# Performance work log

Measured on AMD Instinct MI355X. Metric: run time of the kernel, lower is better.

Reference implementation:

```python
import jax, jax.numpy as jnp
import numpy as np

N = 100000
D = 64
H = 4 * D  # 256
E = 1000000


def setup_inputs() -> dict:
    key = jax.random.key(0)
    ks = jax.random.split(key, 9)
    return {
        "loc_feat": jax.random.normal(ks[0], (N, D), dtype=jnp.float32),
        "geo_src": jax.random.randint(ks[1], (E,), 0, N),
        "geo_dst": jax.random.randint(ks[2], (E,), 0, N),
        "trans_src": jax.random.randint(ks[3], (E,), 0, N),
        "trans_dst": jax.random.randint(ks[4], (E,), 0, N),
        "trans_w": jax.random.uniform(ks[5], (E,), dtype=jnp.float32),
        "W1": jax.random.normal(ks[6], (D, H), dtype=jnp.float32) * (1.0 / np.sqrt(D)),
        "b1": jax.random.normal(ks[7], (H,), dtype=jnp.float32) * 0.01,
        "W2": jax.random.normal(ks[8], (H, 1), dtype=jnp.float32) * (1.0 / np.sqrt(H)),
    }


def reference(loc_feat, geo_src, geo_dst, trans_src, trans_dst, trans_w, W1, b1, W2):
    n = loc_feat.shape[0]
    # etype 'geo': copy_u + mean  -> segment mean of src features at dst
    geo_sum = jax.ops.segment_sum(loc_feat[geo_src], geo_dst, num_segments=n)
    cnt = jax.ops.segment_sum(jnp.ones(geo_src.shape[0], loc_feat.dtype), geo_dst, num_segments=n)
    geo = jnp.where(cnt[:, None] > 0, geo_sum / jnp.maximum(cnt, 1.0)[:, None], 0.0)
    # etype 'trans': u_mul_e + sum -> weighted segment sum
    trans = jax.ops.segment_sum(loc_feat[trans_src] * trans_w[:, None], trans_dst, num_segments=n)
    # semantic attention fuse over the two relation views
    z = jnp.stack([geo, trans], axis=1)          # [N, 2, D]
    h = jnp.tanh(jnp.einsum('nkd,dh->nkh', z, W1) + b1)  # [N, 2, H]
    w = jnp.einsum('nkh,ho->nko', h, W2).mean(0)  # [2, 1] (mean over nodes)
    beta = jax.nn.softmax(w, axis=0)              # [2, 1]
    return (beta[None, :, :] * z).sum(1)          # [N, D]
```

## Files before the change

### kernel.cpp

```cpp
#include <hip/hip_runtime.h>
#include <hip/hip_bf16.h>

#define N_NODES 100000
#define DIM 64
#define HID 256
#define E_EDGES 1000000
#define TWO_N (2 * N_NODES)
#define MLP_ROWBLOCKS (TWO_N / 64)

#define TILE 240
#define NBINS 417
#define CAP 3072
#define EPB 4096
#define GEO_BLOCKS 245

typedef short short8 __attribute__((ext_vector_type(8)));
typedef float f32x4 __attribute__((ext_vector_type(4)));
typedef unsigned short us4 __attribute__((ext_vector_type(4)));

__device__ __forceinline__ float tanh_fast(float x) {
    x = fminf(fmaxf(x, -15.0f), 15.0f);
    float e = __expf(2.0f * x);
    return (e - 1.0f) / (e + 1.0f);
}

__device__ __forceinline__ unsigned short f2bf(float x) {
    unsigned u = __float_as_uint(x);
    u = u + 0x7FFFu + ((u >> 16) & 1u);
    return (unsigned short)(u >> 16);
}

__global__ void pack_feat_kernel(const float* __restrict__ feat,
                                 unsigned short* __restrict__ fb) {
    int i = blockIdx.x * 256 + threadIdx.x;
    float4 v = ((const float4*)feat)[i];
    us4 o;
    o[0] = f2bf(v.x); o[1] = f2bf(v.y); o[2] = f2bf(v.z); o[3] = f2bf(v.w);
    ((us4*)fb)[i] = o;
}

__global__ void bin_fill_kernel(const int* __restrict__ gs, const int* __restrict__ gd,
                                const int* __restrict__ ts, const int* __restrict__ td,
                                const float* __restrict__ tw,
                                int* __restrict__ gcount,
                                int* __restrict__ gbin, int2* __restrict__ tbin) {
    __shared__ int hist[NBINS];
    __shared__ int baseS[NBINS];
    __shared__ int cur[NBINS];
    int t = threadIdx.x;
    int blk = blockIdx.x;
    int rel = (blk >= GEO_BLOCKS) ? 1 : 0;
    int e0 = (rel ? blk - GEO_BLOCKS : blk) * EPB;
    const int* dstp = rel ? td : gd;
    const int* srcp = rel ? ts : gs;

    int dc[16];
    #pragma unroll
    for (int j = 0; j < 4; ++j) {
        int idx = e0 + j * 1024 + 4 * t;
        if (idx + 3 < E_EDGES) {
            int4 v = *(const int4*)&dstp[idx];
            dc[4 * j + 0] = v.x; dc[4 * j + 1] = v.y;
            dc[4 * j + 2] = v.z; dc[4 * j + 3] = v.w;
        } else {
            #pragma unroll
            for (int i2 = 0; i2 < 4; ++i2)
                dc[4 * j + i2] = (idx + i2 < E_EDGES) ? dstp[idx + i2] : -1;
        }
    }

    for (int i = t; i < NBINS; i += 256) { hist[i] = 0; cur[i] = 0; }
    __syncthreads();

    #pragma unroll
    for (int i = 0; i < 16; ++i)
        if (dc[i] >= 0) atomicAdd(&hist[dc[i] / TILE], 1);
    __syncthreads();

    for (int i = t; i < NBINS; i += 256) {
        int h = hist[i];
        baseS[i] = (h > 0) ? (i * CAP + atomicAdd(&gcount[rel * NBINS + i], h)) : 0;
    }
    __syncthreads();

    if (!rel) {
        #pragma unroll
        for (int j = 0; j < 4; ++j) {
            int idx = e0 + j * 1024 + 4 * t;
            bool vec = (idx + 3 < E_EDGES);
            int4 sv = {0, 0, 0, 0};
            if (vec) sv = *(const int4*)&srcp[idx];
            int ss[4] = {sv.x, sv.y, sv.z, sv.w};
            #pragma unroll
            for (int i2 = 0; i2 < 4; ++i2) {
                int d = dc[4 * j + i2];
                if (d < 0) continue;
                int s = vec ? ss[i2] : srcp[idx + i2];
                int bin = d / TILE;
                int pos = atomicAdd(&cur[bin], 1);
                int gi = baseS[bin] + pos;
                if (gi < (bin + 1) * CAP)
                    gbin[gi] = s | ((d - bin * TILE) << 20);
            }
        }
    } else {
        #pragma unroll
        for (int j = 0; j < 4; ++j) {
            int idx = e0 + j * 1024 + 4 * t;
            bool vec = (idx + 3 < E_EDGES);
            int4 sv = {0, 0, 0, 0};
            float4 wv = {0.f, 0.f, 0.f, 0.f};
            if (vec) {
                sv = *(const int4*)&srcp[idx];
                wv = *(const float4*)&tw[idx];
            }
            int ss[4] = {sv.x, sv.y, sv.z, sv.w};
            float ww[4] = {wv.x, wv.y, wv.z, wv.w};
            #pragma unroll
            for (int i2 = 0; i2 < 4; ++i2) {
                int d = dc[4 * j + i2];
                if (d < 0) continue;
                int s = vec ? ss[i2] : srcp[idx + i2];
                float w = vec ? ww[i2] : tw[idx + i2];
                int bin = d / TILE;
                int pos = atomicAdd(&cur[bin], 1);
                int gi = baseS[bin] + pos;
                if (gi < (bin + 1) * CAP)
                    tbin[gi] = make_int2(s | ((d - bin * TILE) << 20), __float_as_int(w));
            }
        }
    }
}

__global__ void __launch_bounds__(512) aggregate_kernel(
        const unsigned short* __restrict__ featb,
        const int* __restrict__ gbin, const int2* __restrict__ tbin,
        const int* __restrict__ gcount,
        float* __restrict__ out_geo, float* __restrict__ trans_out,
        int* __restrict__ cnt_out) {
    __shared__ int   srcS[CAP];
    __shared__ float wS[CAP];
    __shared__ int   histS[TILE];
    __shared__ int   baseS[TILE];
    __shared__ int   curS[TILE];
    __shared__ int   scanS[256];

    int b = blockIdx.x;
    int rel = (b >= NBINS) ? 1 : 0;
    int bin = rel ? b - NBINS : b;
    int node0 = bin * TILE;
    int nNodes = min(TILE, N_NODES - node0);
    int t = threadIdx.x, lane = t & 63, wave = t >> 6;
    int half = lane >> 5, hl = lane & 31;

    int nE = gcount[b];
    if (nE > CAP) nE = CAP;

    for (int i = t; i < TILE; i += 512) histS[i] = 0;
    __syncthreads();

    if (!rel) {
        const int* bp = gbin + (size_t)bin * CAP;
        for (int i = t; i < nE; i += 512) atomicAdd(&histS[bp[i] >> 20], 1);
    } else {
        const int2* bp = tbin + (size_t)bin * CAP;
        for (int i = t; i < nE; i += 512) atomicAdd(&histS[bp[i].x >> 20], 1);
    }
    __syncthreads();

    if (t < 256) scanS[t] = (t < TILE) ? histS[t] : 0;
    __syncthreads();
    #pragma unroll
    for (int off = 1; off < 256; off <<= 1) {
        int add = 0;
        if (t < 256 && t >= off) add = scanS[t - off];
        __syncthreads();
        if (t < 256) scanS[t] += add;
        __syncthreads();
    }
    if (t < TILE) {
        int base = scanS[t] - histS[t];
        baseS[t] = base;
        curS[t] = base;
    }
    __syncthreads();

    if (!rel) {
        const int* bp = gbin + (size_t)bin * CAP;
        for (int i = t; i < nE; i += 512) {
            int p = bp[i];
            int pos = atomicAdd(&curS[p >> 20], 1);
            srcS[pos] = p & 0xFFFFF;
        }
    } else {
        const int2* bp = tbin + (size_t)bin * CAP;
        for (int i = t; i < nE; i += 512) {
            int2 p = bp[i];
            int pos = atomicAdd(&curS[p.x >> 20], 1);
            srcS[pos] = p.x & 0xFFFFF;
            wS[pos] = __int_as_float(p.y);
        }
    }
    __syncthreads();

    for (int nl = wave; nl < nNodes; nl += 8) {
        int deg = histS[nl];
        int base = baseS[nl];
        float ax = 0.0f, ay = 0.0f;
        if (!rel) {
            int k = 0;
            for (; k + 7 < deg; k += 8) {
                int s0 = srcS[base + k + half];
                int s1 = srcS[base + k + 2 + half];
                int s2 = srcS[base + k + 4 + half];
                int s3 = srcS[base + k + 6 + half];
                unsigned r0 = *(const unsigned*)&featb[(size_t)s0 * DIM + 2 * hl];
                unsigned r1 = *(const unsigned*)&featb[(size_t)s1 * DIM + 2 * hl];
                unsigned r2 = *(const unsigned*)&featb[(size_t)s2 * DIM + 2 * hl];
                unsigned r3 = *(const unsigned*)&featb[(size_t)s3 * DIM + 2 * hl];
                ax += __uint_as_float(r0 << 16) + __uint_as_float(r1 << 16)
                    + __uint_as_float(r2 << 16) + __uint_as_float(r3 << 16);
                ay += __uint_as_float(r0 & 0xFFFF0000u) + __uint_as_float(r1 & 0xFFFF0000u)
                    + __uint_as_float(r2 & 0xFFFF0000u) + __uint_as_float(r3 & 0xFFFF0000u);
            }
            for (; k + 1 < deg; k += 2) {
                int s = srcS[base + k + half];
                unsigned r = *(const unsigned*)&featb[(size_t)s * DIM + 2 * hl];
                ax += __uint_as_float(r << 16);
                ay += __uint_as_float(r & 0xFFFF0000u);
            }
            if (k < deg && half == 0) {
                int s = srcS[base + k];
                unsigned r = *(const unsigned*)&featb[(size_t)s * DIM + 2 * hl];
                ax += __uint_as_float(r << 16);
                ay += __uint_as_float(r & 0xFFFF0000u);
            }
        } else {
            int k = 0;
            for (; k + 7 < deg; k += 8) {
                int s0 = srcS[base + k + half];
                int s1 = srcS[base + k + 2 + half];
                int s2 = srcS[base + k + 4 + half];
                int s3 = srcS[base + k + 6 + half];
                float w0 = wS[base + k + half];
                float w1 = wS[base + k + 2 + half];
                float w2 = wS[base + k + 4 + half];
                float w3 = wS[base + k + 6 + half];
                unsigned r0 = *(const unsigned*)&featb[(size_t)s0 * DIM + 2 * hl];
                unsigned r1 = *(const unsigned*)&featb[(size_t)s1 * DIM + 2 * hl];
                unsigned r2 = *(const unsigned*)&featb[(size_t)s2 * DIM + 2 * hl];
                unsigned r3 = *(const unsigned*)&featb[(size_t)s3 * DIM + 2 * hl];
                ax += __uint_as_float(r0 << 16) * w0 + __uint_as_float(r1 << 16) * w1
                    + __uint_as_float(r2 << 16) * w2 + __uint_as_float(r3 << 16) * w3;
                ay += __uint_as_float(r0 & 0xFFFF0000u) * w0 + __uint_as_float(r1 & 0xFFFF0000u) * w1
                    + __uint_as_float(r2 & 0xFFFF0000u) * w2 + __uint_as_float(r3 & 0xFFFF0000u) * w3;
            }
            for (; k + 1 < deg; k += 2) {
                int s = srcS[base + k + half];
                float w = wS[base + k + half];
                unsigned r = *(const unsigned*)&featb[(size_t)s * DIM + 2 * hl];
                ax += __uint_as_float(r << 16) * w;
                ay += __uint_as_float(r & 0xFFFF0000u) * w;
            }
            if (k < deg && half == 0) {
                int s = srcS[base + k];
                float w = wS[base + k];
                unsigned r = *(const unsigned*)&featb[(size_t)s * DIM + 2 * hl];
                ax += __uint_as_float(r << 16) * w;
                ay += __uint_as_float(r & 0xFFFF0000u) * w;
            }
        }
        ax += __shfl_down(ax, 32);
        ay += __shfl_down(ay, 32);
        if (half == 0) {
            float* outp = (rel ? trans_out : out_geo) + (size_t)(node0 + nl) * DIM + 2 * hl;
            float2 o; o.x = ax; o.y = ay;
            *(float2*)outp = o;
        }
    }
    if (!rel && t < nNodes) cnt_out[node0 + t] = histS[t];
}

__global__ void pack_w1_kernel(const float* __restrict__ W1, unsigned short* __restrict__ W1p) {
    int i = blockIdx.x * 256 + threadIdx.x;
    int j = i & 7;
    int r = i >> 3;
    int nidx = r & 15; r >>= 4;
    int q = r & 3; r >>= 2;
    int khalf = r & 1;
    int n = r >> 1;
    int k = 32 * khalf + 8 * q + j;
    int c = 16 * n + nidx;
    W1p[i] = f2bf(W1[k * HID + c]);
}

__global__ void __launch_bounds__(256) mlp_mfma_kernel(
        const float* __restrict__ geo_raw, const float* __restrict__ trans,
        const int* __restrict__ cnt,
        const unsigned short* __restrict__ W1p,
        const float* __restrict__ bias1, const float* __restrict__ W2,
        float* __restrict__ partials) {
    __shared__ float wred[4][2];
    int t = threadIdx.x, lane = t & 63, wave = t >> 6;
    int m = lane & 15, q = lane >> 4;
    int base = blockIdx.x * 64 + wave * 16;
    int R = base + m;

    const float* rowp;
    float scale;
    if (R < N_NODES) {
        rowp = geo_raw + (size_t)R * DIM;
        scale = 1.0f / fmaxf((float)cnt[R], 1.0f);
    } else {
        rowp = trans + (size_t)(R - N_NODES) * DIM;
        scale = 1.0f;
    }

    float4 v0 = *(const float4*)(rowp + q * 8);
    float4 v1 = *(const float4*)(rowp + q * 8 + 4);
    float4 v2 = *(const float4*)(rowp + 32 + q * 8);
    float4 v3 = *(const float4*)(rowp + 32 + q * 8 + 4);
    short8 a0, a1;
    a0[0] = (short)f2bf(v0.x * scale); a0[1] = (short)f2bf(v0.y * scale);
    a0[2] = (short)f2bf(v0.z * scale); a0[3] = (short)f2bf(v0.w * scale);
    a0[4] = (short)f2bf(v1.x * scale); a0[5] = (short)f2bf(v1.y * scale);
    a0[6] = (short)f2bf(v1.z * scale); a0[7] = (short)f2bf(v1.w * scale);
    a1[0] = (short)f2bf(v2.x * scale); a1[1] = (short)f2bf(v2.y * scale);
    a1[2] = (short)f2bf(v2.z * scale); a1[3] = (short)f2bf(v2.w * scale);
    a1[4] = (short)f2bf(v3.x * scale); a1[5] = (short)f2bf(v3.y * scale);
    a1[6] = (short)f2bf(v3.z * scale); a1[7] = (short)f2bf(v3.w * scale);

    float c0 = 0.0f, c1 = 0.0f;
    const short8* W1v = (const short8*)W1p;

    #pragma unroll 4
    for (int n = 0; n < 16; ++n) {
        short8 b0 = W1v[(n * 2 + 0) * 64 + lane];
        short8 bK = W1v[(n * 2 + 1) * 64 + lane];
        f32x4 acc = {0.0f, 0.0f, 0.0f, 0.0f};
        acc = __builtin_amdgcn_mfma_f32_16x16x32_bf16(a0, b0, acc, 0, 0, 0);
        acc = __builtin_amdgcn_mfma_f32_16x16x32_bf16(a1, bK, acc, 0, 0, 0);
        int col = 16 * n + m;
        float bj = bias1[col];
        float w2 = W2[col];
        #pragma unroll
        for (int reg = 0; reg < 4; ++reg) {
            int Rr = base + q * 4 + reg;
            float h = tanh_fast(acc[reg] + bj);
            float contrib = h * w2;
            if (Rr < N_NODES) c0 += contrib; else c1 += contrib;
        }
    }

    #pragma unroll
    for (int off = 32; off > 0; off >>= 1) {
        c0 += __shfl_down(c0, off);
        c1 += __shfl_down(c1, off);
    }
    if (lane == 0) { wred[wave][0] = c0; wred[wave][1] = c1; }
    __syncthreads();
    if (t == 0) {
        partials[blockIdx.x * 2 + 0] = wred[0][0] + wred[1][0] + wred[2][0] + wred[3][0];
        partials[blockIdx.x * 2 + 1] = wred[0][1] + wred[1][1] + wred[2][1] + wred[3][1];
    }
}

__global__ void beta_kernel(const float* __restrict__ partials, float* __restrict__ beta) {
    __shared__ float wred[4][2];
    int t = threadIdx.x;
    float c0 = 0.0f, c1 = 0.0f;
    for (int i = t; i < MLP_ROWBLOCKS; i += 256) {
        c0 += partials[i * 2 + 0];
        c1 += partials[i * 2 + 1];
    }
    #pragma unroll
    for (int off = 32; off > 0; off >>= 1) {
        c0 += __shfl_down(c0, off);
        c1 += __shfl_down(c1, off);
    }
    int lane = t & 63, wv = t >> 6;
    if (lane == 0) { wred[wv][0] = c0; wred[wv][1] = c1; }
    __syncthreads();
    if (t == 0) {
        float s0 = (wred[0][0] + wred[1][0] + wred[2][0] + wred[3][0]) / (float)N_NODES;
        float s1 = (wred[0][1] + wred[1][1] + wred[2][1] + wred[3][1]) / (float)N_NODES;
        float m = fmaxf(s0, s1);
        float e0 = __expf(s0 - m), e1 = __expf(s1 - m);
        float inv = 1.0f / (e0 + e1);
        beta[0] = e0 * inv;
        beta[1] = e1 * inv;
    }
}

__global__ void combine_kernel(float* __restrict__ out_geo,
                               const float* __restrict__ trans,
                               const int* __restrict__ cnt,
                               const float* __restrict__ beta) {
    int gid = blockIdx.x * 256 + threadIdx.x;
    int node = gid >> 4;
    float invc = 1.0f / fmaxf((float)cnt[node], 1.0f);
    float b0 = beta[0] * invc;
    float b1 = beta[1];
    float4 g = ((const float4*)out_geo)[gid];
    float4 tr = ((const float4*)trans)[gid];
    float4 o;
    o.x = b0 * g.x + b1 * tr.x;
    o.y = b0 * g.y + b1 * tr.y;
    o.z = b0 * g.z + b1 * tr.z;
    o.w = b0 * g.w + b1 * tr.w;
    ((float4*)out_geo)[gid] = o;
}

extern "C" void kernel_launch(void* const* d_in, const int* in_sizes, int n_in,
                              void* d_out, int out_size, void* d_ws, size_t ws_size,
                              hipStream_t stream) {
    const float* loc_feat = (const float*)d_in[0];
    const int* geo_src    = (const int*)d_in[1];
    const int* geo_dst    = (const int*)d_in[2];
    const int* trans_src  = (const int*)d_in[3];
    const int* trans_dst  = (const int*)d_in[4];
    const float* trans_w  = (const float*)d_in[5];
    const float* W1       = (const float*)d_in[6];
    const float* b1       = (const float*)d_in[7];
    const float* W2       = (const float*)d_in[8];
    float* out = (float*)d_out;

    float* trans    = (float*)d_ws;
    int*   cnt      = (int*)(trans + (size_t)N_NODES * DIM);
    int*   gcount   = cnt + N_NODES;
    int*   gbin     = gcount + 2 * NBINS;
    int2*  tbin     = (int2*)(gbin + (size_t)NBINS * CAP);
    float* partials = (float*)(tbin + (size_t)NBINS * CAP);
    float* beta     = partials + 2 * MLP_ROWBLOCKS;
    unsigned short* W1p   = (unsigned short*)(beta + 2);
    unsigned short* featb = W1p + 16384;

    hipMemsetAsync(gcount, 0, 2 * NBINS * sizeof(int), stream);

    pack_feat_kernel<<<(N_NODES * DIM / 4) / 256, 256, 0, stream>>>(loc_feat, featb);
    pack_w1_kernel<<<64, 256, 0, stream>>>(W1, W1p);
    bin_fill_kernel<<<2 * GEO_BLOCKS, 256, 0, stream>>>(geo_src, geo_dst, trans_src,
                                                        trans_dst, trans_w,
                                                        gcount, gbin, tbin);
    aggregate_kernel<<<2 * NBINS, 512, 0, stream>>>(featb, gbin, tbin, gcount,
                                                    out, trans, cnt);
    mlp_mfma_kernel<<<MLP_ROWBLOCKS, 256, 0, stream>>>(out, trans, cnt, W1p, b1, W2, partials);
    beta_kernel<<<1, 256, 0, stream>>>(partials, beta);
    combine_kernel<<<(N_NODES * DIM / 4) / 256, 256, 0, stream>>>(out, trans, cnt, beta);
}
```

Measured before the change: 252.0 us.

## Store aggregated views as bf16 z buffer and widen gather loads

The aggregate kernel now applies the mean scaling itself and writes geo and trans rows as a single bf16 buffer. The MLP and combine kernels then read bf16 directly instead of fp32 plus counts, which cuts intermediate traffic and removes conversion work in the MLP. The gather now loads 8 bytes per lane with 4 edges per wave iteration. Binning uses 8192 edges per block and recomputes histograms without register staging. Rounding the z values to bf16 adds some precision loss to the output combine.

Measured after the change: 247.7 us. No clear change (-1.7%).

```diff
diff --git a/kernel.cpp b/kernel.cpp
--- a/kernel.cpp
+++ b/kernel.cpp
@@ -11,8 +11,8 @@
 #define TILE 240
 #define NBINS 417
 #define CAP 3072
-#define EPB 4096
-#define GEO_BLOCKS 245
+#define EPB 8192
+#define GEO_BLOCKS 123
 
 typedef short short8 __attribute__((ext_vector_type(8)));
 typedef float f32x4 __attribute__((ext_vector_type(4)));
@@ -28,6 +28,10 @@
     unsigned u = __float_as_uint(x);
     u = u + 0x7FFFu + ((u >> 16) & 1u);
     return (unsigned short)(u >> 16);
+}
+
+__device__ __forceinline__ float bf2f(unsigned short u) {
+    return __uint_as_float(((unsigned)u) << 16);
 }
 
 __global__ void pack_feat_kernel(const float* __restrict__ feat,
@@ -54,27 +58,23 @@
     const int* dstp = rel ? td : gd;
     const int* srcp = rel ? ts : gs;
 
-    int dc[16];
+    for (int i = t; i < NBINS; i += 256) { hist[i] = 0; cur[i] = 0; }
+    __syncthreads();
+
     #pragma unroll
-    for (int j = 0; j < 4; ++j) {
+    for (int j = 0; j < EPB / 1024; ++j) {
         int idx = e0 + j * 1024 + 4 * t;
         if (idx + 3 < E_EDGES) {
             int4 v = *(const int4*)&dstp[idx];
-            dc[4 * j + 0] = v.x; dc[4 * j + 1] = v.y;
-            dc[4 * j + 2] = v.z; dc[4 * j + 3] = v.w;
+            atomicAdd(&hist[v.x / TILE], 1);
+            atomicAdd(&hist[v.y / TILE], 1);
+            atomicAdd(&hist[v.z / TILE], 1);
+            atomicAdd(&hist[v.w / TILE], 1);
         } else {
-            #pragma unroll
             for (int i2 = 0; i2 < 4; ++i2)
-                dc[4 * j + i2] = (idx + i2 < E_EDGES) ? dstp[idx + i2] : -1;
-        }
-    }
-
-    for (int i = t; i < NBINS; i += 256) { hist[i] = 0; cur[i] = 0; }
-    __syncthreads();
-
-    #pragma unroll
-    for (int i = 0; i < 16; ++i)
-        if (dc[i] >= 0) atomicAdd(&hist[dc[i] / TILE], 1);
+                if (idx + i2 < E_EDGES) atomicAdd(&hist[dstp[idx + i2] / TILE], 1);
+        }
+    }
     __syncthreads();
 
     for (int i = t; i < NBINS; i += 256) {
@@ -85,48 +85,52 @@
 
     if (!rel) {
         #pragma unroll
-        for (int j = 0; j < 4; ++j) {
+        for (int j = 0; j < EPB / 1024; ++j) {
             int idx = e0 + j * 1024 + 4 * t;
             bool vec = (idx + 3 < E_EDGES);
-            int4 sv = {0, 0, 0, 0};
-            if (vec) sv = *(const int4*)&srcp[idx];
+            int4 dv, sv;
+            if (vec) { dv = *(const int4*)&dstp[idx]; sv = *(const int4*)&srcp[idx]; }
+            int dd[4] = {dv.x, dv.y, dv.z, dv.w};
             int ss[4] = {sv.x, sv.y, sv.z, sv.w};
-            #pragma unroll
             for (int i2 = 0; i2 < 4; ++i2) {
-                int d = dc[4 * j + i2];
-                if (d < 0) continue;
-                int s = vec ? ss[i2] : srcp[idx + i2];
+                if (!vec) {
+                    if (idx + i2 >= E_EDGES) continue;
+                    dd[i2] = dstp[idx + i2]; ss[i2] = srcp[idx + i2];
+                }
+                int d = dd[i2];
                 int bin = d / TILE;
                 int pos = atomicAdd(&cur[bin], 1);
                 int gi = baseS[bin] + pos;
                 if (gi < (bin + 1) * CAP)
-                    gbin[gi] = s | ((d - bin * TILE) << 20);
+                    gbin[gi] = ss[i2] | ((d - bin * TILE) << 20);
             }
         }
     } else {
         #pragma unroll
-        for (int j = 0; j < 4; ++j) {
+        for (int j = 0; j < EPB / 1024; ++j) {
             int idx = e0 + j * 1024 + 4 * t;
             bool vec = (idx + 3 < E_EDGES);
-            int4 sv = {0, 0, 0, 0};
-            float4 wv = {0.f, 0.f, 0.f, 0.f};
+            int4 dv, sv; float4 wv;
             if (vec) {
+                dv = *(const int4*)&dstp[idx];
                 sv = *(const int4*)&srcp[idx];
                 wv = *(const float4*)&tw[idx];
             }
+            int dd[4] = {dv.x, dv.y, dv.z, dv.w};
             int ss[4] = {sv.x, sv.y, sv.z, sv.w};
             float ww[4] = {wv.x, wv.y, wv.z, wv.w};
-            #pragma unroll
             for (int i2 = 0; i2 < 4; ++i2) {
-                int d = dc[4 * j + i2];
-                if (d < 0) continue;
-                int s = vec ? ss[i2] : srcp[idx + i2];
-                float w = vec ? ww[i2] : tw[idx + i2];
+                if (!vec) {
+                    if (idx + i2 >= E_EDGES) continue;
+                    dd[i2] = dstp[idx + i2]; ss[i2] = srcp[idx + i2]; ww[i2] = tw[idx + i2];
+                }
+                int d = dd[i2];
                 int bin = d / TILE;
                 int pos = atomicAdd(&cur[bin], 1);
                 int gi = baseS[bin] + pos;
                 if (gi < (bin + 1) * CAP)
-                    tbin[gi] = make_int2(s | ((d - bin * TILE) << 20), __float_as_int(w));
+                    tbin[gi] = make_int2(ss[i2] | ((d - bin * TILE) << 20),
+                                         __float_as_int(ww[i2]));
             }
         }
     }
@@ -136,8 +140,7 @@
         const unsigned short* __restrict__ featb,
         const int* __restrict__ gbin, const int2* __restrict__ tbin,
         const int* __restrict__ gcount,
-        float* __restrict__ out_geo, float* __restrict__ trans_out,
-        int* __restrict__ cnt_out) {
+        unsigned short* __restrict__ zb) {
     __shared__ int   srcS[CAP];
     __shared__ float wS[CAP];
     __shared__ int   histS[TILE];
@@ -151,7 +154,7 @@
     int node0 = bin * TILE;
     int nNodes = min(TILE, N_NODES - node0);
     int t = threadIdx.x, lane = t & 63, wave = t >> 6;
-    int half = lane >> 5, hl = lane & 31;
+    int q = lane >> 4, ql = lane & 15;
 
     int nE = gcount[b];
     if (nE > CAP) nE = CAP;
@@ -206,79 +209,66 @@
     for (int nl = wave; nl < nNodes; nl += 8) {
         int deg = histS[nl];
         int base = baseS[nl];
-        float ax = 0.0f, ay = 0.0f;
+        float a0 = 0.f, a1 = 0.f, a2 = 0.f, a3 = 0.f;
         if (!rel) {
             int k = 0;
             for (; k + 7 < deg; k += 8) {
-                int s0 = srcS[base + k + half];
-                int s1 = srcS[base + k + 2 + half];
-                int s2 = srcS[base + k + 4 + half];
-                int s3 = srcS[base + k + 6 + half];
-                unsigned r0 = *(const unsigned*)&featb[(size_t)s0 * DIM + 2 * hl];
-                unsigned r1 = *(const unsigned*)&featb[(size_t)s1 * DIM + 2 * hl];
-                unsigned r2 = *(const unsigned*)&featb[(size_t)s2 * DIM + 2 * hl];
-                unsigned r3 = *(const unsigned*)&featb[(size_t)s3 * DIM + 2 * hl];
-                ax += __uint_as_float(r0 << 16) + __uint_as_float(r1 << 16)
-                    + __uint_as_float(r2 << 16) + __uint_as_float(r3 << 16);
-                ay += __uint_as_float(r0 & 0xFFFF0000u) + __uint_as_float(r1 & 0xFFFF0000u)
-                    + __uint_as_float(r2 & 0xFFFF0000u) + __uint_as_float(r3 & 0xFFFF0000u);
-            }
-            for (; k + 1 < deg; k += 2) {
-                int s = srcS[base + k + half];
-                unsigned r = *(const unsigned*)&featb[(size_t)s * DIM + 2 * hl];
-                ax += __uint_as_float(r << 16);
-                ay += __uint_as_float(r & 0xFFFF0000u);
-            }
-            if (k < deg && half == 0) {
-                int s = srcS[base + k];
-                unsigned r = *(const unsigned*)&featb[(size_t)s * DIM + 2 * hl];
-                ax += __uint_as_float(r << 16);
-                ay += __uint_as_float(r & 0xFFFF0000u);
+                int s0 = srcS[base + k + q];
+                int s1 = srcS[base + k + 4 + q];
+                us4 r0 = *(const us4*)&featb[(size_t)s0 * DIM + ql * 4];
+                us4 r1 = *(const us4*)&featb[(size_t)s1 * DIM + ql * 4];
+                a0 += bf2f(r0[0]) + bf2f(r1[0]);
+                a1 += bf2f(r0[1]) + bf2f(r1[1]);
+                a2 += bf2f(r0[2]) + bf2f(r1[2]);
+                a3 += bf2f(r0[3]) + bf2f(r1[3]);
+            }
+            for (; k < deg; k += 4) {
+                int e = k + q;
+                if (e < deg) {
+                    int s = srcS[base + e];
+                    us4 r = *(const us4*)&featb[(size_t)s * DIM + ql * 4];
+                    a0 += bf2f(r[0]); a1 += bf2f(r[1]);
+                    a2 += bf2f(r[2]); a3 += bf2f(r[3]);
+                }
             }
         } else {
             int k = 0;
             for (; k + 7 < deg; k += 8) {
-                int s0 = srcS[base + k + half];
-                int s1 = srcS[base + k + 2 + half];
-                int s2 = srcS[base + k + 4 + half];
-                int s3 = srcS[base + k + 6 + half];
-                float w0 = wS[base + k + half];
-                float w1 = wS[base + k + 2 + half];
-                float w2 = wS[base + k + 4 + half];
-                float w3 = wS[base + k + 6 + half];
-                unsigned r0 = *(const unsigned*)&featb[(size_t)s0 * DIM + 2 * hl];
-                unsigned r1 = *(const unsigned*)&featb[(size_t)s1 * DIM + 2 * hl];
-                unsigned r2 = *(const unsigned*)&featb[(size_t)s2 * DIM + 2 * hl];
-                unsigned r3 = *(const unsigned*)&featb[(size_t)s3 * DIM + 2 * hl];
-                ax += __uint_as_float(r0 << 16) * w0 + __uint_as_float(r1 << 16) * w1
-                    + __uint_as_float(r2 << 16) * w2 + __uint_as_float(r3 << 16) * w3;
-                ay += __uint_as_float(r0 & 0xFFFF0000u) * w0 + __uint_as_float(r1 & 0xFFFF0000u) * w1
-                    + __uint_as_float(r2 & 0xFFFF0000u) * w2 + __uint_as_float(r3 & 0xFFFF0000u) * w3;
-            }
-            for (; k + 1 < deg; k += 2) {
-                int s = srcS[base + k + half];
-                float w = wS[base + k + half];
-                unsigned r = *(const unsigned*)&featb[(size_t)s * DIM + 2 * hl];
-                ax += __uint_as_float(r << 16) * w;
-                ay += __uint_as_float(r & 0xFFFF0000u) * w;
-            }
-            if (k < deg && half == 0) {
-                int s = srcS[base + k];
-                float w = wS[base + k];
-                unsigned r = *(const unsigned*)&featb[(size_t)s * DIM + 2 * hl];
-                ax += __uint_as_float(r << 16) * w;
-                ay += __uint_as_float(r & 0xFFFF0000u) * w;
-            }
-        }
-        ax += __shfl_down(ax, 32);
-        ay += __shfl_down(ay, 32);
-        if (half == 0) {
-            float* outp = (rel ? trans_out : out_geo) + (size_t)(node0 + nl) * DIM + 2 * hl;
-            float2 o; o.x = ax; o.y = ay;
-            *(float2*)outp = o;
-        }
-    }
-    if (!rel && t < nNodes) cnt_out[node0 + t] = histS[t];
+                int s0 = srcS[base + k + q];
+                int s1 = srcS[base + k + 4 + q];
+                float w0 = wS[base + k + q];
+                float w1 = wS[base + k + 4 + q];
+                us4 r0 = *(const us4*)&featb[(size_t)s0 * DIM + ql * 4];
+                us4 r1 = *(const us4*)&featb[(size_t)s1 * DIM + ql * 4];
+                a0 += bf2f(r0[0]) * w0 + bf2f(r1[0]) * w1;
+                a1 += bf2f(r0[1]) * w0 + bf2f(r1[1]) * w1;
+                a2 += bf2f(r0[2]) * w0 + bf2f(r1[2]) * w1;
+                a3 += bf2f(r0[3]) * w0 + bf2f(r1[3]) * w1;
+            }
+            for (; k < deg; k += 4) {
+                int e = k + q;
+                if (e < deg) {
+                    int s = srcS[base + e];
+                    float w = wS[base + e];
+                    us4 r = *(const us4*)&featb[(size_t)s * DIM + ql * 4];
+                    a0 += bf2f(r[0]) * w; a1 += bf2f(r[1]) * w;
+                    a2 += bf2f(r[2]) * w; a3 += bf2f(r[3]) * w;
+                }
+            }
+        }
+        a0 += __shfl_down(a0, 16); a1 += __shfl_down(a1, 16);
+        a2 += __shfl_down(a2, 16); a3 += __shfl_down(a3, 16);
+        a0 += __shfl_down(a0, 32); a1 += __shfl_down(a1, 32);
+        a2 += __shfl_down(a2, 32); a3 += __shfl_down(a3, 32);
+        if (lane < 16) {
+            float sc = rel ? 1.0f : 1.0f / fmaxf((float)deg, 1.0f);
+            us4 o;
+            o[0] = f2bf(a0 * sc); o[1] = f2bf(a1 * sc);
+            o[2] = f2bf(a2 * sc); o[3] = f2bf(a3 * sc);
+            size_t row = (size_t)(rel ? N_NODES + node0 + nl : node0 + nl);
+            *(us4*)&zb[row * DIM + ql * 4] = o;
+        }
+    }
 }
 
 __global__ void pack_w1_kernel(const float* __restrict__ W1, unsigned short* __restrict__ W1p) {
@@ -295,8 +285,7 @@
 }
 
 __global__ void __launch_bounds__(256) mlp_mfma_kernel(
-        const float* __restrict__ geo_raw, const float* __restrict__ trans,
-        const int* __restrict__ cnt,
+        const unsigned short* __restrict__ zb,
         const unsigned short* __restrict__ W1p,
         const float* __restrict__ bias1, const float* __restrict__ W2,
         float* __restrict__ partials) {
@@ -306,29 +295,9 @@
     int base = blockIdx.x * 64 + wave * 16;
     int R = base + m;
 
-    const float* rowp;
-    float scale;
-    if (R < N_NODES) {
-        rowp = geo_raw + (size_t)R * DIM;
-        scale = 1.0f / fmaxf((float)cnt[R], 1.0f);
-    } else {
-        rowp = trans + (size_t)(R - N_NODES) * DIM;
-        scale = 1.0f;
-    }
-
-    float4 v0 = *(const float4*)(rowp + q * 8);
-    float4 v1 = *(const float4*)(rowp + q * 8 + 4);
-    float4 v2 = *(const float4*)(rowp + 32 + q * 8);
-    float4 v3 = *(const float4*)(rowp + 32 + q * 8 + 4);
-    short8 a0, a1;
-    a0[0] = (short)f2bf(v0.x * scale); a0[1] = (short)f2bf(v0.y * scale);
-    a0[2] = (short)f2bf(v0.z * scale); a0[3] = (short)f2bf(v0.w * scale);
-    a0[4] = (short)f2bf(v1.x * scale); a0[5] = (short)f2bf(v1.y * scale);
-    a0[6] = (short)f2bf(v1.z * scale); a0[7] = (short)f2bf(v1.w * scale);
-    a1[0] = (short)f2bf(v2.x * scale); a1[1] = (short)f2bf(v2.y * scale);
-    a1[2] = (short)f2bf(v2.z * scale); a1[3] = (short)f2bf(v2.w * scale);
-    a1[4] = (short)f2bf(v3.x * scale); a1[5] = (short)f2bf(v3.y * scale);
-    a1[6] = (short)f2bf(v3.z * scale); a1[7] = (short)f2bf(v3.w * scale);
+    const unsigned short* rowp = zb + (size_t)R * DIM;
+    short8 a0 = *(const short8*)(rowp + q * 8);
+    short8 a1 = *(const short8*)(rowp + 32 + q * 8);
 
     float c0 = 0.0f, c1 = 0.0f;
     const short8* W1v = (const short8*)W1p;
@@ -392,23 +361,25 @@
     }
 }
 
-__global__ void combine_kernel(float* __restrict__ out_geo,
-                               const float* __restrict__ trans,
-                               const int* __restrict__ cnt,
-                               const float* __restrict__ beta) {
+__global__ void combine_kernel(const unsigned short* __restrict__ zb,
+                               const float* __restrict__ beta,
+                               float* __restrict__ out) {
     int gid = blockIdx.x * 256 + threadIdx.x;
-    int node = gid >> 4;
-    float invc = 1.0f / fmaxf((float)cnt[node], 1.0f);
-    float b0 = beta[0] * invc;
+    float b0 = beta[0];
     float b1 = beta[1];
-    float4 g = ((const float4*)out_geo)[gid];
-    float4 tr = ((const float4*)trans)[gid];
-    float4 o;
-    o.x = b0 * g.x + b1 * tr.x;
-    o.y = b0 * g.y + b1 * tr.y;
-    o.z = b0 * g.z + b1 * tr.z;
-    o.w = b0 * g.w + b1 * tr.w;
-    ((float4*)out_geo)[gid] = o;
+    uint4 g = *(const uint4*)&zb[(size_t)gid * 8];
+    uint4 tr = *(const uint4*)&zb[(size_t)N_NODES * DIM + (size_t)gid * 8];
+    float4 o0, o1;
+    o0.x = b0 * __uint_as_float(g.x << 16) + b1 * __uint_as_float(tr.x << 16);
+    o0.y = b0 * __uint_as_float(g.x & 0xFFFF0000u) + b1 * __uint_as_float(tr.x & 0xFFFF0000u);
+    o0.z = b0 * __uint_as_float(g.y << 16) + b1 * __uint_as_float(tr.y << 16);
+    o0.w = b0 * __uint_as_float(g.y & 0xFFFF0000u) + b1 * __uint_as_float(tr.y & 0xFFFF0000u);
+    o1.x = b0 * __uint_as_float(g.z << 16) + b1 * __uint_as_float(tr.z << 16);
+    o1.y = b0 * __uint_as_float(g.z & 0xFFFF0000u) + b1 * __uint_as_float(tr.z & 0xFFFF0000u);
+    o1.z = b0 * __uint_as_float(g.w << 16) + b1 * __uint_as_float(tr.w << 16);
+    o1.w = b0 * __uint_as_float(g.w & 0xFFFF0000u) + b1 * __uint_as_float(tr.w & 0xFFFF0000u);
+    *(float4*)&out[(size_t)gid * 8] = o0;
+    *(float4*)&out[(size_t)gid * 8 + 4] = o1;
 }
 
 extern "C" void kernel_launch(void* const* d_in, const int* in_sizes, int n_in,
@@ -425,15 +396,14 @@
     const float* W2       = (const float*)d_in[8];
     float* out = (float*)d_out;
 
-    float* trans    = (float*)d_ws;
-    int*   cnt      = (int*)(trans + (size_t)N_NODES * DIM);
-    int*   gcount   = cnt + N_NODES;
+    int*   gcount   = (int*)d_ws;
     int*   gbin     = gcount + 2 * NBINS;
     int2*  tbin     = (int2*)(gbin + (size_t)NBINS * CAP);
     float* partials = (float*)(tbin + (size_t)NBINS * CAP);
     float* beta     = partials + 2 * MLP_ROWBLOCKS;
     unsigned short* W1p   = (unsigned short*)(beta + 2);
     unsigned short* featb = W1p + 16384;
+    unsigned short* zb    = featb + (size_t)N_NODES * DIM;
 
     hipMemsetAsync(gcount, 0, 2 * NBINS * sizeof(int), stream);
 
@@ -442,9 +412,8 @@
     bin_fill_kernel<<<2 * GEO_BLOCKS, 256, 0, stream>>>(geo_src, geo_dst, trans_src,
                                                         trans_dst, trans_w,
                                                         gcount, gbin, tbin);
-    aggregate_kernel<<<2 * NBINS, 512, 0, stream>>>(featb, gbin, tbin, gcount,
-                                                    out, trans, cnt);
-    mlp_mfma_kernel<<<MLP_ROWBLOCKS, 256, 0, stream>>>(out, trans, cnt, W1p, b1, W2, partials);
+    aggregate_kernel<<<2 * NBINS, 512, 0, stream>>>(featb, gbin, tbin, gcount, zb);
+    mlp_mfma_kernel<<<MLP_ROWBLOCKS, 256, 0, stream>>>(zb, W1p, b1, W2, partials);
     beta_kernel<<<1, 256, 0, stream>>>(partials, beta);
-    combine_kernel<<<(N_NODES * DIM / 4) / 256, 256, 0, stream>>>(out, trans, cnt, beta);
-}
+    combine_kernel<<<(N_NODES * DIM / 8) / 256, 256, 0, stream>>>(zb, beta, out);
+}
```
